# Performance work log

Measured on AMD Instinct MI355X. Metric: run time of the kernel, lower is better.

Reference implementation:

```python
import jax, jax.numpy as jnp
import numpy as np

N_NODES = 100000
N_EDGES = 1600000
N_FEAT = 128
N_CLASSES = 10
N_GRAPHS = 256


def setup_inputs() -> dict:
    key = jax.random.key(0)
    ks = jax.random.split(key, 16)
    x = jax.random.normal(ks[0], (N_NODES, N_FEAT), dtype=jnp.float32)
    edge_index = jax.random.randint(ks[1], (2, N_EDGES), 0, N_NODES, dtype=jnp.int64)
    batch = jnp.sort(jax.random.randint(ks[2], (N_NODES,), 0, N_GRAPHS, dtype=jnp.int64))
    s = 0.1
    # GAT1: in=128 -> heads=8, out_per_head=8, concat -> 64
    W1 = jax.random.normal(ks[3], (N_FEAT, 64), dtype=jnp.float32) * s
    a_src1 = jax.random.normal(ks[4], (8, 8), dtype=jnp.float32) * s
    a_dst1 = jax.random.normal(ks[5], (8, 8), dtype=jnp.float32) * s
    b1 = jnp.zeros((64,), jnp.float32)
    # GAT2: in=64 -> heads=1, out=128
    W2 = jax.random.normal(ks[6], (64, 128), dtype=jnp.float32) * s
    a_src2 = jax.random.normal(ks[7], (1, 128), dtype=jnp.float32) * s
    a_dst2 = jax.random.normal(ks[8], (1, 128), dtype=jnp.float32) * s
    b2 = jnp.zeros((128,), jnp.float32)
    fc_w = jax.random.normal(ks[9], (128, N_CLASSES), dtype=jnp.float32) * s
    fc_b = jnp.zeros((N_CLASSES,), jnp.float32)
    return {"x": x, "edge_index": edge_index, "batch": batch,
            "W1": W1, "a_src1": a_src1, "a_dst1": a_dst1, "b1": b1,
            "W2": W2, "a_src2": a_src2, "a_dst2": a_dst2, "b2": b2,
            "fc_w": fc_w, "fc_b": fc_b}


def _segment_softmax(e, seg, n):
    # e: [E, H]; softmax over edges sharing the same destination node
    m = jax.ops.segment_max(e, seg, num_segments=n)
    m = jnp.where(jnp.isfinite(m), m, jnp.zeros_like(m))  # guard isolated nodes
    ex = jnp.exp(e - m[seg])
    s = jax.ops.segment_sum(ex, seg, num_segments=n)
    return ex / (s[seg] + jnp.asarray(1e-16, e.dtype))


def _gat_conv(x, src, dst, W, a_src, a_dst, bias):
    # PyG GATConv (eval mode, self-loops already appended to src/dst)
    H, C = a_src.shape
    n = x.shape[0]
    h = (x @ W).reshape(n, H, C)                      # [N,H,C]
    al_s = jnp.einsum('nhc,hc->nh', h, a_src)          # [N,H]
    al_d = jnp.einsum('nhc,hc->nh', h, a_dst)
    e = jax.nn.leaky_relu(al_s[src] + al_d[dst], 0.2)  # [E,H]
    alpha = _segment_softmax(e, dst, n)                # [E,H]
    out = jax.ops.segment_sum(h[src] * alpha[..., None], dst, num_segments=n)  # [N,H,C]
    return out.reshape(n, H * C) + bias                # concat=True (H=1 layer2 is identity reshape)


def reference(x, edge_index, batch, W1, a_src1, a_dst1, b1, W2, a_src2, a_dst2, b2, fc_w, fc_b):
    n = x.shape[0]
    loop = jnp.arange(n, dtype=edge_index.dtype)
    src = jnp.concatenate([edge_index[0], loop])       # add self-loops (PyG default)
    dst = jnp.concatenate([edge_index[1], loop])
    x1 = jax.nn.relu(_gat_conv(x, src, dst, W1, a_src1, a_dst1, b1))
    # dropout p=0.6 is identity in eval mode
    x2 = _gat_conv(x1, src, dst, W2, a_src2, a_dst2, b2)
    cnt = jax.ops.segment_sum(jnp.ones((n,), x2.dtype), batch, num_segments=N_GRAPHS)
    pooled = jax.ops.segment_sum(x2, batch, num_segments=N_GRAPHS) / jnp.maximum(cnt, 1.0)[:, None]
    logits = pooled @ fc_w + fc_b
    return jax.nn.log_softmax(logits, axis=1)
```

## Files before the change

### kernel.cpp

```cpp
#include <hip/hip_runtime.h>
#include <math.h>

typedef unsigned int uint;
typedef unsigned short ushort;
typedef unsigned char uchar;
typedef __attribute__((ext_vector_type(2))) float v2f;

#define S1 4.0f
#define S2 16.0f

template <bool HI>
__device__ inline v2f fp8x2f(uint u) {
    return __builtin_amdgcn_cvt_pk_f32_fp8((int)u, HI);
}

__global__ __launch_bounds__(256) void k_gemm1(const float* __restrict__ x,
                                               const float* __restrict__ W1,
                                               const float* __restrict__ as1,
                                               const float* __restrict__ ad1,
                                               uchar* __restrict__ h1f8,
                                               float* __restrict__ al1s,
                                               float* __restrict__ al1d, int N) {
    __shared__ float sB[128 * 64];
    __shared__ float sA[64 * 68];
    const int t = threadIdx.x;
    const int n0 = blockIdx.x * 64;
    {
        const float4* w4 = (const float4*)W1;
        float4* s4 = (float4*)sB;
#pragma unroll
        for (int i = 0; i < 8; ++i) s4[t + i * 256] = w4[t + i * 256];
    }
    const int r0 = (t >> 3) * 2;
    const int c0 = (t & 7) * 8;
    float acc0[8] = {0, 0, 0, 0, 0, 0, 0, 0};
    float acc1[8] = {0, 0, 0, 0, 0, 0, 0, 0};
    for (int kb = 0; kb < 2; ++kb) {
        __syncthreads();
#pragma unroll
        for (int i = 0; i < 4; ++i) {
            int idx = t + i * 256;
            int r = idx >> 4, kc = idx & 15;
            int n = n0 + r;
            float4 v = make_float4(0.f, 0.f, 0.f, 0.f);
            if (n < N) v = ((const float4*)x)[(size_t)n * 32 + kb * 16 + kc];
            *(float4*)&sA[r * 68 + kc * 4] = v;
        }
        __syncthreads();
        const float* bptr = &sB[kb * 64 * 64];
#pragma unroll 8
        for (int kk = 0; kk < 64; ++kk) {
            float a0 = sA[r0 * 68 + kk];
            float a1 = sA[(r0 + 1) * 68 + kk];
            const float* bp = &bptr[kk * 64 + c0];
            float4 b0 = *(const float4*)bp;
            float4 b1v = *(const float4*)(bp + 4);
            acc0[0] += a0 * b0.x; acc0[1] += a0 * b0.y; acc0[2] += a0 * b0.z; acc0[3] += a0 * b0.w;
            acc0[4] += a0 * b1v.x; acc0[5] += a0 * b1v.y; acc0[6] += a0 * b1v.z; acc0[7] += a0 * b1v.w;
            acc1[0] += a1 * b0.x; acc1[1] += a1 * b0.y; acc1[2] += a1 * b0.z; acc1[3] += a1 * b0.w;
            acc1[4] += a1 * b1v.x; acc1[5] += a1 * b1v.y; acc1[6] += a1 * b1v.z; acc1[7] += a1 * b1v.w;
        }
    }
    float ps0 = 0.f, pd0 = 0.f, ps1 = 0.f, pd1 = 0.f;
#pragma unroll
    for (int i = 0; i < 8; ++i) {
        float ws = as1[c0 + i], wd = ad1[c0 + i];
        ps0 += acc0[i] * ws; pd0 += acc0[i] * wd;
        ps1 += acc1[i] * ws; pd1 += acc1[i] * wd;
    }
    int n = n0 + r0;
    int head = t & 7;
    if (n < N) {
        int q0 = 0, q1 = 0;
        q0 = __builtin_amdgcn_cvt_pk_fp8_f32(acc0[0] * S1, acc0[1] * S1, q0, false);
        q0 = __builtin_amdgcn_cvt_pk_fp8_f32(acc0[2] * S1, acc0[3] * S1, q0, true);
        q1 = __builtin_amdgcn_cvt_pk_fp8_f32(acc0[4] * S1, acc0[5] * S1, q1, false);
        q1 = __builtin_amdgcn_cvt_pk_fp8_f32(acc0[6] * S1, acc0[7] * S1, q1, true);
        uint2 p; p.x = (uint)q0; p.y = (uint)q1;
        *(uint2*)&h1f8[(size_t)n * 64 + c0] = p;
        al1s[(size_t)n * 8 + head] = ps0;
        al1d[(size_t)n * 8 + head] = pd0;
    }
    if (n + 1 < N) {
        int q0 = 0, q1 = 0;
        q0 = __builtin_amdgcn_cvt_pk_fp8_f32(acc1[0] * S1, acc1[1] * S1, q0, false);
        q0 = __builtin_amdgcn_cvt_pk_fp8_f32(acc1[2] * S1, acc1[3] * S1, q0, true);
        q1 = __builtin_amdgcn_cvt_pk_fp8_f32(acc1[4] * S1, acc1[5] * S1, q1, false);
        q1 = __builtin_amdgcn_cvt_pk_fp8_f32(acc1[6] * S1, acc1[7] * S1, q1, true);
        uint2 p; p.x = (uint)q0; p.y = (uint)q1;
        *(uint2*)&h1f8[(size_t)(n + 1) * 64 + c0] = p;
        al1s[(size_t)(n + 1) * 8 + head] = ps1;
        al1d[(size_t)(n + 1) * 8 + head] = pd1;
    }
}

__global__ __launch_bounds__(256) void k_gemm2(const float* __restrict__ x1pre,
                                               const float* __restrict__ W2,
                                               const float* __restrict__ b1,
                                               const float* __restrict__ as2,
                                               const float* __restrict__ ad2,
                                               uchar* __restrict__ h2f8,
                                               float* __restrict__ al2s,
                                               float* __restrict__ al2d, int N) {
    __shared__ float sB[64 * 128];
    __shared__ float sA[64 * 68];
    const int t = threadIdx.x;
    const int n0 = blockIdx.x * 64;
    {
        const float4* w4 = (const float4*)W2;
        float4* s4 = (float4*)sB;
#pragma unroll
        for (int i = 0; i < 8; ++i) s4[t + i * 256] = w4[t + i * 256];
    }
#pragma unroll
    for (int i = 0; i < 4; ++i) {
        int idx = t + i * 256;
        int r = idx >> 4, kc = idx & 15;
        int n = n0 + r;
        float4 v = make_float4(0.f, 0.f, 0.f, 0.f);
        if (n < N) {
            v = ((const float4*)x1pre)[(size_t)n * 16 + kc];
            float4 bb = ((const float4*)b1)[kc];
            v.x = fmaxf(v.x + bb.x, 0.f);
            v.y = fmaxf(v.y + bb.y, 0.f);
            v.z = fmaxf(v.z + bb.z, 0.f);
            v.w = fmaxf(v.w + bb.w, 0.f);
        }
        *(float4*)&sA[r * 68 + kc * 4] = v;
    }
    __syncthreads();
    const int r0 = (t >> 3) * 2;
    const int cb = (t & 7) * 4;
    float acc0[16], acc1[16];
#pragma unroll
    for (int i = 0; i < 16; ++i) { acc0[i] = 0.f; acc1[i] = 0.f; }
#pragma unroll 4
    for (int k = 0; k < 64; ++k) {
        float a0 = sA[r0 * 68 + k];
        float a1 = sA[(r0 + 1) * 68 + k];
#pragma unroll
        for (int j = 0; j < 4; ++j) {
            float4 b = *(const float4*)&sB[k * 128 + cb + 32 * j];
            acc0[j * 4 + 0] += a0 * b.x; acc0[j * 4 + 1] += a0 * b.y;
            acc0[j * 4 + 2] += a0 * b.z; acc0[j * 4 + 3] += a0 * b.w;
            acc1[j * 4 + 0] += a1 * b.x; acc1[j * 4 + 1] += a1 * b.y;
            acc1[j * 4 + 2] += a1 * b.z; acc1[j * 4 + 3] += a1 * b.w;
        }
    }
    float ps0 = 0.f, pd0 = 0.f, ps1 = 0.f, pd1 = 0.f;
#pragma unroll
    for (int j = 0; j < 4; ++j)
#pragma unroll
        for (int i = 0; i < 4; ++i) {
            int cc = cb + 32 * j + i;
            float ws = as2[cc], wd = ad2[cc];
            ps0 += acc0[j * 4 + i] * ws; pd0 += acc0[j * 4 + i] * wd;
            ps1 += acc1[j * 4 + i] * ws; pd1 += acc1[j * 4 + i] * wd;
        }
#pragma unroll
    for (int off = 1; off < 8; off <<= 1) {
        ps0 += __shfl_xor(ps0, off); pd0 += __shfl_xor(pd0, off);
        ps1 += __shfl_xor(ps1, off); pd1 += __shfl_xor(pd1, off);
    }
    int n = n0 + r0;
    if (n < N) {
#pragma unroll
        for (int j = 0; j < 4; ++j) {
            int q = 0;
            q = __builtin_amdgcn_cvt_pk_fp8_f32(acc0[j * 4 + 0] * S2, acc0[j * 4 + 1] * S2, q, false);
            q = __builtin_amdgcn_cvt_pk_fp8_f32(acc0[j * 4 + 2] * S2, acc0[j * 4 + 3] * S2, q, true);
            *(uint*)&h2f8[(size_t)n * 128 + cb + 32 * j] = (uint)q;
        }
        if ((t & 7) == 0) { al2s[n] = ps0; al2d[n] = pd0; }
    }
    if (n + 1 < N) {
#pragma unroll
        for (int j = 0; j < 4; ++j) {
            int q = 0;
            q = __builtin_amdgcn_cvt_pk_fp8_f32(acc1[j * 4 + 0] * S2, acc1[j * 4 + 1] * S2, q, false);
            q = __builtin_amdgcn_cvt_pk_fp8_f32(acc1[j * 4 + 2] * S2, acc1[j * 4 + 3] * S2, q, true);
            *(uint*)&h2f8[(size_t)(n + 1) * 128 + cb + 32 * j] = (uint)q;
        }
        if ((t & 7) == 0) { al2s[n + 1] = ps1; al2d[n + 1] = pd1; }
    }
}


__global__ __launch_bounds__(256) void k_hist(const int* __restrict__ dst,
                                              int* __restrict__ counts,
                                              int E, int CH, int NB) {
    __shared__ int hist[784];
    int t = threadIdx.x, b = blockIdx.x;
    for (int k = t; k < NB; k += 256) hist[k] = 0;
    __syncthreads();
    int e0 = b * CH;
    int e1 = e0 + CH; if (e1 > E) e1 = E;
    for (int e = e0 + t; e < e1; e += 256)
        atomicAdd(&hist[dst[e] >> 7], 1);
    __syncthreads();
    for (int k = t; k < NB; k += 256) counts[(size_t)b * NB + k] = hist[k];
}

__global__ __launch_bounds__(256) void k_bscan(int* __restrict__ counts,
                                               int* __restrict__ btot,
                                               int C, int NB) {
    __shared__ int sh[256];
    int t = threadIdx.x, k = blockIdx.x;
    int v[4];
#pragma unroll
    for (int i = 0; i < 4; ++i) {
        int b = t * 4 + i;
        v[i] = (b < C) ? counts[(size_t)b * NB + k] : 0;
    }
    int s = v[0] + v[1] + v[2] + v[3];
    sh[t] = s;
    __syncthreads();
    int accv = s;
    for (int off = 1; off < 256; off <<= 1) {
        int u = (t >= off) ? sh[t - off] : 0;
        __syncthreads();
        accv += u;
        sh[t] = accv;
        __syncthreads();
    }
    int excl = accv - s;
#pragma unroll
    for (int i = 0; i < 4; ++i) {
        int b = t * 4 + i;
        if (b < C) counts[(size_t)b * NB + k] = excl;
        excl += v[i];
    }
    if (t == 255) btot[k] = accv;
}

__global__ void k_bscan2(const int* __restrict__ btot, int* __restrict__ bbase,
                         int NB, int E) {
    __shared__ int sh[1024];
    int t = threadIdx.x;
    int v = (t < NB) ? btot[t] : 0;
    sh[t] = v;
    __syncthreads();
    int accv = v;
    for (int off = 1; off < 1024; off <<= 1) {
        int u = (t >= off) ? sh[t - off] : 0;
        __syncthreads();
        accv += u;
        sh[t] = accv;
        __syncthreads();
    }
    if (t < NB) bbase[t] = accv - v;
    if (t == 0) bbase[NB] = E;
}

__global__ __launch_bounds__(256) void k_bucket(const int* __restrict__ src,
                                                const int* __restrict__ dst,
                                                const int* __restrict__ counts,
                                                const int* __restrict__ bbase,
                                                int* __restrict__ ebuf,
                                                int E, int CH, int NB) {
    __shared__ int pos[784];
    int t = threadIdx.x, b = blockIdx.x;
    for (int k = t; k < NB; k += 256)
        pos[k] = bbase[k] + counts[(size_t)b * NB + k];
    __syncthreads();
    int e0 = b * CH;
    int e1 = e0 + CH; if (e1 > E) e1 = E;
    for (int e = e0 + t; e < e1; e += 256) {
        int d = dst[e], s = src[e];
        int p = atomicAdd(&pos[d >> 7], 1);
        ebuf[p] = (int)((uint)s | ((uint)(d & 127) << 25));
    }
}

__global__ __launch_bounds__(256) void k_csr(const int* __restrict__ bbase,
                                             const int* __restrict__ ebuf,
                                             int* __restrict__ row_ptr,
                                             int* __restrict__ col,
                                             int N, int E) {
    __shared__ int cnt[128];
    __shared__ int fill[128];
    __shared__ int rowb[128];
    __shared__ int sh[256];
    int t = threadIdx.x, k = blockIdx.x;
    int lo = bbase[k], hi = bbase[k + 1];
    int nlo = k << 7;
    int nn = N - nlo; if (nn > 128) nn = 128;
    if (t < 128) { cnt[t] = 0; fill[t] = 0; }
    __syncthreads();
    for (int i = lo + t; i < hi; i += 256)
        atomicAdd(&cnt[((uint)ebuf[i]) >> 25], 1);
    __syncthreads();
    int v = (t < nn) ? (cnt[t] + 1) : 0;
    sh[t] = v;
    __syncthreads();
    int accv = v;
    for (int off = 1; off < 256; off <<= 1) {
        int u = (t >= off) ? sh[t - off] : 0;
        __syncthreads();
        accv += u;
        sh[t] = accv;
        __syncthreads();
    }
    int fbase = lo + nlo;
    if (t < nn) {
        int rb = fbase + accv - v;
        rowb[t] = rb;
        row_ptr[nlo + t] = rb;
        col[rb + cnt[t]] = nlo + t;
    }
    if (k == 0 && t == 0) row_ptr[N] = E + N;
    __syncthreads();
    for (int i = lo + t; i < hi; i += 256) {
        uint e = (uint)ebuf[i];
        int j = (int)(e >> 25);
        int r = atomicAdd(&fill[j], 1);
        col[rowb[j] + r] = (int)(e & 0x1FFFFFFu);
    }
}

__global__ __launch_bounds__(256) void k_edge1(const uchar* __restrict__ h1f8,
                                               const float* __restrict__ al1s,
                                               const float* __restrict__ al1d,
                                               const int* __restrict__ row_ptr,
                                               const int* __restrict__ col,
                                               float* __restrict__ x1pre, int N) {
    int node = blockIdx.x * 4 + (threadIdx.x >> 6);
    if (node >= N) return;
    const int lane = threadIdx.x & 63;
    const int g = lane >> 4;
    const int k4 = lane & 15;
    const int hh = k4 >> 1;
    const uint co = (uint)(k4 * 4);
    const float a_dh = al1d[(((uint)node) << 3) | (uint)hh];
    const int s0 = row_ptr[node], s1 = row_ptr[node + 1];
    float den_part = 0.f;
    v2f accL = {0.f, 0.f};
    v2f accH = {0.f, 0.f};
    for (int base = s0; base < s1; base += 64) {
        int cnt = s1 - base; if (cnt > 64) cnt = 64;
        int cntR = (cnt + 3) & ~3;
        int i = 0;
        for (; i + 16 <= cntR; i += 16) {
            int eA = base + i + g, eB = eA + 4, eC = eA + 8, eD = eA + 12;
            int xD = eD < s1 ? eD : s1 - 1;
            int cA = col[eA], cB = col[eB], cC = col[eC], cD = col[xD];
            uint hA = *(const uint*)(h1f8 + ((((uint)cA) << 6) | co));
            uint hB = *(const uint*)(h1f8 + ((((uint)cB) << 6) | co));
            uint hC = *(const uint*)(h1f8 + ((((uint)cC) << 6) | co));
            uint hD = *(const uint*)(h1f8 + ((((uint)cD) << 6) | co));
            float lA = al1s[((((uint)cA) << 3) | (uint)hh)] + a_dh;
            float lB = al1s[((((uint)cB) << 3) | (uint)hh)] + a_dh;
            float lC = al1s[((((uint)cC) << 3) | (uint)hh)] + a_dh;
            float lD = al1s[((((uint)cD) << 3) | (uint)hh)] + a_dh;
            lA = lA > 0.f ? lA : 0.2f * lA;
            lB = lB > 0.f ? lB : 0.2f * lB;
            lC = lC > 0.f ? lC : 0.2f * lC;
            lD = lD > 0.f ? lD : 0.2f * lD;
            float wA = __expf(lA);
            float wB = __expf(lB);
            float wC = __expf(lC);
            float wD = (eD < s1) ? __expf(lD) : 0.f;
            den_part += wA + wB + wC + wD;
            v2f wA2 = {wA, wA}, wB2 = {wB, wB}, wC2 = {wC, wC}, wD2 = {wD, wD};
            accL += wA2 * fp8x2f<false>(hA);
            accH += wA2 * fp8x2f<true>(hA);
            accL += wB2 * fp8x2f<false>(hB);
            accH += wB2 * fp8x2f<true>(hB);
            accL += wC2 * fp8x2f<false>(hC);
            accH += wC2 * fp8x2f<true>(hC);
            accL += wD2 * fp8x2f<false>(hD);
            accH += wD2 * fp8x2f<true>(hD);
        }
        int rem = cntR - i;
        if (rem & 8) {
            int eA = base + i + g, eB = eA + 4;
            int xB = eB < s1 ? eB : s1 - 1;
            int cA = col[eA], cB = col[xB];
            uint hA = *(const uint*)(h1f8 + ((((uint)cA) << 6) | co));
            uint hB = *(const uint*)(h1f8 + ((((uint)cB) << 6) | co));
            float lA = al1s[((((uint)cA) << 3) | (uint)hh)] + a_dh;
            float lB = al1s[((((uint)cB) << 3) | (uint)hh)] + a_dh;
            lA = lA > 0.f ? lA : 0.2f * lA;
            lB = lB > 0.f ? lB : 0.2f * lB;
            float wA = __expf(lA);
            float wB = (eB < s1) ? __expf(lB) : 0.f;
            den_part += wA + wB;
            v2f wA2 = {wA, wA}, wB2 = {wB, wB};
            accL += wA2 * fp8x2f<false>(hA);
            accH += wA2 * fp8x2f<true>(hA);
            accL += wB2 * fp8x2f<false>(hB);
            accH += wB2 * fp8x2f<true>(hB);
            i += 8;
        }
        if (rem & 4) {
            int eA = base + i + g;
            int xA = eA < s1 ? eA : s1 - 1;
            int cA = col[xA];
            uint hA = *(const uint*)(h1f8 + ((((uint)cA) << 6) | co));
            float lA = al1s[((((uint)cA) << 3) | (uint)hh)] + a_dh;
            lA = lA > 0.f ? lA : 0.2f * lA;
            float wA = (eA < s1) ? __expf(lA) : 0.f;
            den_part += wA;
            v2f wA2 = {wA, wA};
            accL += wA2 * fp8x2f<false>(hA);
            accH += wA2 * fp8x2f<true>(hA);
        }
    }
    float a0 = accL.x, a1 = accL.y, a2 = accH.x, a3 = accH.y;
    a0 += __shfl_xor(a0, 16); a0 += __shfl_xor(a0, 32);
    a1 += __shfl_xor(a1, 16); a1 += __shfl_xor(a1, 32);
    a2 += __shfl_xor(a2, 16); a2 += __shfl_xor(a2, 32);
    a3 += __shfl_xor(a3, 16); a3 += __shfl_xor(a3, 32);
    den_part += __shfl_xor(den_part, 16);
    den_part += __shfl_xor(den_part, 32);
    if (lane < 16) {
        float invd = 1.f / (den_part * S1);
        ((float4*)x1pre)[(size_t)node * 16 + k4] =
            make_float4(a0 * invd, a1 * invd, a2 * invd, a3 * invd);
    }
}

__global__ __launch_bounds__(256) void k_edge2(const uchar* __restrict__ h2f8,
                                               const float* __restrict__ al2s,
                                               const float* __restrict__ al2d,
                                               const int* __restrict__ row_ptr,
                                               const int* __restrict__ col,
                                               float* __restrict__ x2, int N) {
    int node = blockIdx.x * 4 + (threadIdx.x >> 6);
    if (node >= N) return;
    const int lane = threadIdx.x & 63;
    const int g = lane >> 4;
    const int k8 = lane & 15;
    const uint co = (uint)(k8 * 8);
    const float a_d = al2d[node];
    const int s0 = row_ptr[node], s1 = row_ptr[node + 1];
    v2f acc0 = {0.f, 0.f}, acc1 = {0.f, 0.f}, acc2 = {0.f, 0.f}, acc3 = {0.f, 0.f};
    float den_part = 0.f;
    for (int base = s0; base < s1; base += 64) {
        int cnt = s1 - base; if (cnt > 64) cnt = 64;
        int cntR = (cnt + 3) & ~3;
        int i = 0;
        for (; i + 16 <= cntR; i += 16) {
            int eA = base + i + g, eB = eA + 4, eC = eA + 8, eD = eA + 12;
            int xD = eD < s1 ? eD : s1 - 1;
            int cA = col[eA], cB = col[eB], cC = col[eC], cD = col[xD];
            uint2 hA = *(const uint2*)(h2f8 + ((((uint)cA) << 7) | co));
            uint2 hB = *(const uint2*)(h2f8 + ((((uint)cB) << 7) | co));
            uint2 hC = *(const uint2*)(h2f8 + ((((uint)cC) << 7) | co));
            uint2 hD = *(const uint2*)(h2f8 + ((((uint)cD) << 7) | co));
            float lA = al2s[(uint)cA] + a_d;
            float lB = al2s[(uint)cB] + a_d;
            float lC = al2s[(uint)cC] + a_d;
            float lD = al2s[(uint)cD] + a_d;
            lA = lA > 0.f ? lA : 0.2f * lA;
            lB = lB > 0.f ? lB : 0.2f * lB;
            lC = lC > 0.f ? lC : 0.2f * lC;
            lD = lD > 0.f ? lD : 0.2f * lD;
            float wA = __expf(lA);
            float wB = __expf(lB);
            float wC = __expf(lC);
            float wD = (eD < s1) ? __expf(lD) : 0.f;
            den_part += wA + wB + wC + wD;
            v2f wA2 = {wA, wA}, wB2 = {wB, wB}, wC2 = {wC, wC}, wD2 = {wD, wD};
            acc0 += wA2 * fp8x2f<false>(hA.x);
            acc1 += wA2 * fp8x2f<true>(hA.x);
            acc2 += wA2 * fp8x2f<false>(hA.y);
            acc3 += wA2 * fp8x2f<true>(hA.y);
            acc0 += wB2 * fp8x2f<false>(hB.x);
            acc1 += wB2 * fp8x2f<true>(hB.x);
            acc2 += wB2 * fp8x2f<false>(hB.y);
            acc3 += wB2 * fp8x2f<true>(hB.y);
            acc0 += wC2 * fp8x2f<false>(hC.x);
            acc1 += wC2 * fp8x2f<true>(hC.x);
            acc2 += wC2 * fp8x2f<false>(hC.y);
            acc3 += wC2 * fp8x2f<true>(hC.y);
            acc0 += wD2 * fp8x2f<false>(hD.x);
            acc1 += wD2 * fp8x2f<true>(hD.x);
            acc2 += wD2 * fp8x2f<false>(hD.y);
            acc3 += wD2 * fp8x2f<true>(hD.y);
        }
        int rem = cntR - i;
        if (rem & 8) {
            int eA = base + i + g, eB = eA + 4;
            int xB = eB < s1 ? eB : s1 - 1;
            int cA = col[eA], cB = col[xB];
            uint2 hA = *(const uint2*)(h2f8 + ((((uint)cA) << 7) | co));
            uint2 hB = *(const uint2*)(h2f8 + ((((uint)cB) << 7) | co));
            float lA = al2s[(uint)cA] + a_d;
            float lB = al2s[(uint)cB] + a_d;
            lA = lA > 0.f ? lA : 0.2f * lA;
            lB = lB > 0.f ? lB : 0.2f * lB;
            float wA = __expf(lA);
            float wB = (eB < s1) ? __expf(lB) : 0.f;
            den_part += wA + wB;
            v2f wA2 = {wA, wA}, wB2 = {wB, wB};
            acc0 += wA2 * fp8x2f<false>(hA.x);
            acc1 += wA2 * fp8x2f<true>(hA.x);
            acc2 += wA2 * fp8x2f<false>(hA.y);
            acc3 += wA2 * fp8x2f<true>(hA.y);
            acc0 += wB2 * fp8x2f<false>(hB.x);
            acc1 += wB2 * fp8x2f<true>(hB.x);
            acc2 += wB2 * fp8x2f<false>(hB.y);
            acc3 += wB2 * fp8x2f<true>(hB.y);
            i += 8;
        }
        if (rem & 4) {
            int eA = base + i + g;
            int xA = eA < s1 ? eA : s1 - 1;
            int cA = col[xA];
            uint2 hA = *(const uint2*)(h2f8 + ((((uint)cA) << 7) | co));
            float lA = al2s[(uint)cA] + a_d;
            lA = lA > 0.f ? lA : 0.2f * lA;
            float wA = (eA < s1) ? __expf(lA) : 0.f;
            den_part += wA;
            v2f wA2 = {wA, wA};
            acc0 += wA2 * fp8x2f<false>(hA.x);
            acc1 += wA2 * fp8x2f<true>(hA.x);
            acc2 += wA2 * fp8x2f<false>(hA.y);
            acc3 += wA2 * fp8x2f<true>(hA.y);
        }
    }
    den_part += __shfl_xor(den_part, 16);
    den_part += __shfl_xor(den_part, 32);
    float r0 = acc0.x, r1 = acc0.y, r2 = acc1.x, r3 = acc1.y;
    float r4 = acc2.x, r5 = acc2.y, r6 = acc3.x, r7 = acc3.y;
    r0 += __shfl_xor(r0, 16); r0 += __shfl_xor(r0, 32);
    r1 += __shfl_xor(r1, 16); r1 += __shfl_xor(r1, 32);
    r2 += __shfl_xor(r2, 16); r2 += __shfl_xor(r2, 32);
    r3 += __shfl_xor(r3, 16); r3 += __shfl_xor(r3, 32);
    r4 += __shfl_xor(r4, 16); r4 += __shfl_xor(r4, 32);
    r5 += __shfl_xor(r5, 16); r5 += __shfl_xor(r5, 32);
    r6 += __shfl_xor(r6, 16); r6 += __shfl_xor(r6, 32);
    r7 += __shfl_xor(r7, 16); r7 += __shfl_xor(r7, 32);
    if (lane < 16) {
        float invd = 1.f / (den_part * S2);
        float4* dst = (float4*)(x2 + (size_t)node * 128 + co);
        dst[0] = make_float4(r0 * invd, r1 * invd, r2 * invd, r3 * invd);
        dst[1] = make_float4(r4 * invd, r5 * invd, r6 * invd, r7 * invd);
    }
}

__global__ __launch_bounds__(128) void k_pool(const float* __restrict__ x2,
                                              const int* __restrict__ batch,
                                              float* __restrict__ pooled,
                                              float* __restrict__ cnt, int N) {
    int t = threadIdx.x;
    int nstart = blockIdx.x * 128;
    if (nstart >= N) return;
    int nend = nstart + 128;
    if (nend > N) nend = N;
    float acc = 0.f;
    int cur = batch[nstart];
    int count = 0;
    for (int n = nstart; n < nend; ++n) {
        int g = batch[n];
        if (g != cur) {
            atomicAdd(&pooled[(size_t)cur * 128 + t], acc);
            if (t == 0) atomicAdd(&cnt[cur], (float)count);
            acc = 0.f;
            count = 0;
            cur = g;
        }
        acc += x2[(size_t)n * 128 + t];
        ++count;
    }
    atomicAdd(&pooled[(size_t)cur * 128 + t], acc);
    if (t == 0) atomicAdd(&cnt[cur], (float)count);
}

__global__ __launch_bounds__(64) void k_fc(const float* __restrict__ pooled,
                                           const float* __restrict__ cnt,
                                           const float* __restrict__ b2,
                                           const float* __restrict__ fcw,
                                           const float* __restrict__ fcb,
                                           float* __restrict__ out, int G) {
    int g = blockIdx.x;
    int c = threadIdx.x;
    float2 p = ((const float2*)pooled)[(size_t)g * 64 + c];
    float2 bb = ((const float2*)b2)[c];
    float inv = 1.f / fmaxf(cnt[g], 1.f);
    p.x = p.x * inv + bb.x;
    p.y = p.y * inv + bb.y;
    float l[10];
#pragma unroll
    for (int j = 0; j < 10; ++j)
        l[j] = p.x * fcw[(2 * c) * 10 + j] + p.y * fcw[(2 * c + 1) * 10 + j];
#pragma unroll
    for (int j = 0; j < 10; ++j)
        for (int off = 1; off < 64; off <<= 1) l[j] += __shfl_xor(l[j], off);
    if (c == 0) {
        float lj[10];
        float m = -1e30f;
#pragma unroll
        for (int j = 0; j < 10; ++j) {
            lj[j] = l[j] + fcb[j];
            m = fmaxf(m, lj[j]);
        }
        float s = 0.f;
#pragma unroll
        for (int j = 0; j < 10; ++j) s += expf(lj[j] - m);
        float ls = logf(s);
#pragma unroll
        for (int j = 0; j < 10; ++j) out[(size_t)g * 10 + j] = lj[j] - m - ls;
    }
}

extern "C" void kernel_launch(void* const* d_in, const int* in_sizes, int n_in,
                              void* d_out, int out_size, void* d_ws, size_t ws_size,
                              hipStream_t stream) {
    const float* x     = (const float*)d_in[0];
    const int*   ei    = (const int*)d_in[1];
    const int*   batch = (const int*)d_in[2];
    const float* W1    = (const float*)d_in[3];
    const float* as1   = (const float*)d_in[4];
    const float* ad1   = (const float*)d_in[5];
    const float* b1    = (const float*)d_in[6];
    const float* W2    = (const float*)d_in[7];
    const float* as2   = (const float*)d_in[8];
    const float* ad2   = (const float*)d_in[9];
    const float* b2    = (const float*)d_in[10];
    const float* fcw   = (const float*)d_in[11];
    const float* fcb   = (const float*)d_in[12];
    float* out = (float*)d_out;

    const int N = in_sizes[0] / 128;
    const int E = in_sizes[1] / 2;
    const int G = out_size / 10;
    const int* srcp = ei;
    const int* dstp = ei + E;

    float* wf = (float*)d_ws;
    uchar* h1f8   = (uchar*)wf;
    float* x1pre  = wf + (size_t)N * 16;
    float* x2     = wf;
    uchar* h2f8   = (uchar*)(wf + (size_t)N * 128);
    float* al1s_  = wf + (size_t)N * 160;
    float* al1d_  = wf + (size_t)N * 168;
    float* al2s_  = wf + (size_t)N * 176;
    float* al2d_  = wf + (size_t)N * 177;
    float* pooled = wf + (size_t)N * 178;
    float* cnt    = pooled + (size_t)G * 128;

    const int NB = (N + 127) >> 7;
    const int C  = 1024;
    const int CH = (E + C - 1) / C;

    int* ib = (int*)(((uintptr_t)(cnt + G) + 15) & ~(uintptr_t)15);
    int* ebuf    = ib;
    int* counts  = ib + (size_t)E;
    int* btot    = counts + (size_t)C * NB;
    int* bbase   = btot + NB;
    int* row_ptr = bbase + NB + 1;
    int* col     = row_ptr + N + 1;

    size_t zbytes = ((size_t)G * 128 + G) * sizeof(float);
    (void)hipMemsetAsync(pooled, 0, zbytes, stream);

    const int nb64 = (N + 63) / 64;
    const int nb4  = (N + 3) / 4;
    const int nbP  = (N + 127) / 128;

    k_hist<<<C, 256, 0, stream>>>(dstp, counts, E, CH, NB);
    k_gemm1<<<nb64, 256, 0, stream>>>(x, W1, as1, ad1, h1f8, al1s_, al1d_, N);
    k_bscan<<<NB, 256, 0, stream>>>(counts, btot, C, NB);
    k_bscan2<<<1, 1024, 0, stream>>>(btot, bbase, NB, E);
    k_bucket<<<C, 256, 0, stream>>>(srcp, dstp, counts, bbase, ebuf, E, CH, NB);
    k_csr<<<NB, 256, 0, stream>>>(bbase, ebuf, row_ptr, col, N, E);
    k_edge1<<<nb4, 256, 0, stream>>>(h1f8, al1s_, al1d_, row_ptr, col, x1pre, N);
    k_gemm2<<<nb64, 256, 0, stream>>>(x1pre, W2, b1, as2, ad2, h2f8, al2s_, al2d_, N);
    k_edge2<<<nb4, 256, 0, stream>>>(h2f8, al2s_, al2d_, row_ptr, col, x2, N);
    k_pool<<<nbP, 128, 0, stream>>>(x2, batch, pooled, cnt, N);
    k_fc<<<G, 64, 0, stream>>>(pooled, cnt, b2, fcw, fcb, out, G);
}
```

Measured before the change: 351.2 us.

## Interleave layer-1 features with attention logits, fuse bucket scan, store fp16 intermediates

Packs the fp8 layer-1 features and per-head source/destination logits into one 128-byte record per node, so each edge gather in the first attention pass touches a single cache line instead of two separate arrays. The single-block bucket-base scan is folded into every k_bucket block, which removes one kernel launch at the cost of redundant scan work in each block. Layer outputs x1pre and x2 are stored as fp16 instead of fp32, halving their write and read traffic in exchange for some precision loss.

Measured after the change: 340.9 us. 2.9% less time.

```diff
diff --git a/kernel.cpp b/kernel.cpp
--- a/kernel.cpp
+++ b/kernel.cpp
@@ -5,6 +5,8 @@
 typedef unsigned short ushort;
 typedef unsigned char uchar;
 typedef __attribute__((ext_vector_type(2))) float v2f;
+typedef __attribute__((ext_vector_type(4))) _Float16 h4v;
+typedef __attribute__((ext_vector_type(8))) _Float16 h8v;
 
 #define S1 4.0f
 #define S2 16.0f
@@ -18,9 +20,7 @@
                                                const float* __restrict__ W1,
                                                const float* __restrict__ as1,
                                                const float* __restrict__ ad1,
-                                               uchar* __restrict__ h1f8,
-                                               float* __restrict__ al1s,
-                                               float* __restrict__ al1d, int N) {
+                                               uchar* __restrict__ rec1, int N) {
     __shared__ float sB[128 * 64];
     __shared__ float sA[64 * 68];
     const int t = threadIdx.x;
@@ -77,9 +77,10 @@
         q1 = __builtin_amdgcn_cvt_pk_fp8_f32(acc0[4] * S1, acc0[5] * S1, q1, false);
         q1 = __builtin_amdgcn_cvt_pk_fp8_f32(acc0[6] * S1, acc0[7] * S1, q1, true);
         uint2 p; p.x = (uint)q0; p.y = (uint)q1;
-        *(uint2*)&h1f8[(size_t)n * 64 + c0] = p;
-        al1s[(size_t)n * 8 + head] = ps0;
-        al1d[(size_t)n * 8 + head] = pd0;
+        uchar* rp = rec1 + (size_t)n * 128;
+        *(uint2*)(rp + c0) = p;
+        *(float*)(rp + 64 + head * 4) = ps0;
+        *(float*)(rp + 96 + head * 4) = pd0;
     }
     if (n + 1 < N) {
         int q0 = 0, q1 = 0;
@@ -88,13 +89,14 @@
         q1 = __builtin_amdgcn_cvt_pk_fp8_f32(acc1[4] * S1, acc1[5] * S1, q1, false);
         q1 = __builtin_amdgcn_cvt_pk_fp8_f32(acc1[6] * S1, acc1[7] * S1, q1, true);
         uint2 p; p.x = (uint)q0; p.y = (uint)q1;
-        *(uint2*)&h1f8[(size_t)(n + 1) * 64 + c0] = p;
-        al1s[(size_t)(n + 1) * 8 + head] = ps1;
-        al1d[(size_t)(n + 1) * 8 + head] = pd1;
-    }
-}
-
-__global__ __launch_bounds__(256) void k_gemm2(const float* __restrict__ x1pre,
+        uchar* rp = rec1 + (size_t)(n + 1) * 128;
+        *(uint2*)(rp + c0) = p;
+        *(float*)(rp + 64 + head * 4) = ps1;
+        *(float*)(rp + 96 + head * 4) = pd1;
+    }
+}
+
+__global__ __launch_bounds__(256) void k_gemm2(const _Float16* __restrict__ x1pre,
                                                const float* __restrict__ W2,
                                                const float* __restrict__ b1,
                                                const float* __restrict__ as2,
@@ -119,12 +121,12 @@
         int n = n0 + r;
         float4 v = make_float4(0.f, 0.f, 0.f, 0.f);
         if (n < N) {
-            v = ((const float4*)x1pre)[(size_t)n * 16 + kc];
+            h4v hv = *(const h4v*)(x1pre + (size_t)n * 64 + kc * 4);
             float4 bb = ((const float4*)b1)[kc];
-            v.x = fmaxf(v.x + bb.x, 0.f);
-            v.y = fmaxf(v.y + bb.y, 0.f);
-            v.z = fmaxf(v.z + bb.z, 0.f);
-            v.w = fmaxf(v.w + bb.w, 0.f);
+            v.x = fmaxf((float)hv[0] + bb.x, 0.f);
+            v.y = fmaxf((float)hv[1] + bb.y, 0.f);
+            v.z = fmaxf((float)hv[2] + bb.z, 0.f);
+            v.w = fmaxf((float)hv[3] + bb.w, 0.f);
         }
         *(float4*)&sA[r * 68 + kc * 4] = v;
     }
@@ -233,42 +235,55 @@
     if (t == 255) btot[k] = accv;
 }
 
-__global__ void k_bscan2(const int* __restrict__ btot, int* __restrict__ bbase,
-                         int NB, int E) {
-    __shared__ int sh[1024];
-    int t = threadIdx.x;
-    int v = (t < NB) ? btot[t] : 0;
-    sh[t] = v;
-    __syncthreads();
-    int accv = v;
-    for (int off = 1; off < 1024; off <<= 1) {
+__global__ __launch_bounds__(256) void k_bucket(const int* __restrict__ src,
+                                                const int* __restrict__ dst,
+                                                const int* __restrict__ counts,
+                                                const int* __restrict__ btot,
+                                                int* __restrict__ bbase,
+                                                int* __restrict__ ebuf,
+                                                int E, int CH, int NB) {
+    __shared__ int pos[784];
+    __shared__ int sh[256];
+    __shared__ int bb[784];
+    int t = threadIdx.x, b = blockIdx.x;
+    int v[4];
+#pragma unroll
+    for (int i = 0; i < 4; ++i) {
+        int k = t * 4 + i;
+        v[i] = (k < NB) ? btot[k] : 0;
+    }
+    int s = v[0] + v[1] + v[2] + v[3];
+    sh[t] = s;
+    __syncthreads();
+    int accv = s;
+    for (int off = 1; off < 256; off <<= 1) {
         int u = (t >= off) ? sh[t - off] : 0;
         __syncthreads();
         accv += u;
         sh[t] = accv;
         __syncthreads();
     }
-    if (t < NB) bbase[t] = accv - v;
-    if (t == 0) bbase[NB] = E;
-}
-
-__global__ __launch_bounds__(256) void k_bucket(const int* __restrict__ src,
-                                                const int* __restrict__ dst,
-                                                const int* __restrict__ counts,
-                                                const int* __restrict__ bbase,
-                                                int* __restrict__ ebuf,
-                                                int E, int CH, int NB) {
-    __shared__ int pos[784];
-    int t = threadIdx.x, b = blockIdx.x;
+    int excl = accv - s;
+#pragma unroll
+    for (int i = 0; i < 4; ++i) {
+        int k = t * 4 + i;
+        if (k < NB) bb[k] = excl;
+        excl += v[i];
+    }
+    __syncthreads();
     for (int k = t; k < NB; k += 256)
-        pos[k] = bbase[k] + counts[(size_t)b * NB + k];
+        pos[k] = bb[k] + counts[(size_t)b * NB + k];
+    if (b == 0) {
+        for (int k = t; k < NB; k += 256) bbase[k] = bb[k];
+        if (t == 0) bbase[NB] = E;
+    }
     __syncthreads();
     int e0 = b * CH;
     int e1 = e0 + CH; if (e1 > E) e1 = E;
     for (int e = e0 + t; e < e1; e += 256) {
-        int d = dst[e], s = src[e];
+        int d = dst[e], s2 = src[e];
         int p = atomicAdd(&pos[d >> 7], 1);
-        ebuf[p] = (int)((uint)s | ((uint)(d & 127) << 25));
+        ebuf[p] = (int)((uint)s2 | ((uint)(d & 127) << 25));
     }
 }
 
@@ -318,12 +333,10 @@
     }
 }
 
-__global__ __launch_bounds__(256) void k_edge1(const uchar* __restrict__ h1f8,
-                                               const float* __restrict__ al1s,
-                                               const float* __restrict__ al1d,
+__global__ __launch_bounds__(256) void k_edge1(const uchar* __restrict__ rec1,
                                                const int* __restrict__ row_ptr,
                                                const int* __restrict__ col,
-                                               float* __restrict__ x1pre, int N) {
+                                               _Float16* __restrict__ x1pre, int N) {
     int node = blockIdx.x * 4 + (threadIdx.x >> 6);
     if (node >= N) return;
     const int lane = threadIdx.x & 63;
@@ -331,7 +344,8 @@
     const int k4 = lane & 15;
     const int hh = k4 >> 1;
     const uint co = (uint)(k4 * 4);
-    const float a_dh = al1d[(((uint)node) << 3) | (uint)hh];
+    const uint ao = 64u + (uint)(hh * 4);
+    const float a_dh = *(const float*)(rec1 + (((size_t)node) << 7) + 96 + hh * 4);
     const int s0 = row_ptr[node], s1 = row_ptr[node + 1];
     float den_part = 0.f;
     v2f accL = {0.f, 0.f};
@@ -344,14 +358,18 @@
             int eA = base + i + g, eB = eA + 4, eC = eA + 8, eD = eA + 12;
             int xD = eD < s1 ? eD : s1 - 1;
             int cA = col[eA], cB = col[eB], cC = col[eC], cD = col[xD];
-            uint hA = *(const uint*)(h1f8 + ((((uint)cA) << 6) | co));
-            uint hB = *(const uint*)(h1f8 + ((((uint)cB) << 6) | co));
-            uint hC = *(const uint*)(h1f8 + ((((uint)cC) << 6) | co));
-            uint hD = *(const uint*)(h1f8 + ((((uint)cD) << 6) | co));
-            float lA = al1s[((((uint)cA) << 3) | (uint)hh)] + a_dh;
-            float lB = al1s[((((uint)cB) << 3) | (uint)hh)] + a_dh;
-            float lC = al1s[((((uint)cC) << 3) | (uint)hh)] + a_dh;
-            float lD = al1s[((((uint)cD) << 3) | (uint)hh)] + a_dh;
+            const uchar* rA = rec1 + (((uint)cA) << 7);
+            const uchar* rB = rec1 + (((uint)cB) << 7);
+            const uchar* rC = rec1 + (((uint)cC) << 7);
+            const uchar* rD = rec1 + (((uint)cD) << 7);
+            uint hA = *(const uint*)(rA + co);
+            uint hB = *(const uint*)(rB + co);
+            uint hC = *(const uint*)(rC + co);
+            uint hD = *(const uint*)(rD + co);
+            float lA = *(const float*)(rA + ao) + a_dh;
+            float lB = *(const float*)(rB + ao) + a_dh;
+            float lC = *(const float*)(rC + ao) + a_dh;
+            float lD = *(const float*)(rD + ao) + a_dh;
             lA = lA > 0.f ? lA : 0.2f * lA;
             lB = lB > 0.f ? lB : 0.2f * lB;
             lC = lC > 0.f ? lC : 0.2f * lC;
@@ -376,10 +394,12 @@
             int eA = base + i + g, eB = eA + 4;
             int xB = eB < s1 ? eB : s1 - 1;
             int cA = col[eA], cB = col[xB];
-            uint hA = *(const uint*)(h1f8 + ((((uint)cA) << 6) | co));
-            uint hB = *(const uint*)(h1f8 + ((((uint)cB) << 6) | co));
-            float lA = al1s[((((uint)cA) << 3) | (uint)hh)] + a_dh;
-            float lB = al1s[((((uint)cB) << 3) | (uint)hh)] + a_dh;
+            const uchar* rA = rec1 + (((uint)cA) << 7);
+            const uchar* rB = rec1 + (((uint)cB) << 7);
+            uint hA = *(const uint*)(rA + co);
+            uint hB = *(const uint*)(rB + co);
+            float lA = *(const float*)(rA + ao) + a_dh;
+            float lB = *(const float*)(rB + ao) + a_dh;
             lA = lA > 0.f ? lA : 0.2f * lA;
             lB = lB > 0.f ? lB : 0.2f * lB;
             float wA = __expf(lA);
@@ -396,8 +416,9 @@
             int eA = base + i + g;
             int xA = eA < s1 ? eA : s1 - 1;
             int cA = col[xA];
-            uint hA = *(const uint*)(h1f8 + ((((uint)cA) << 6) | co));
-            float lA = al1s[((((uint)cA) << 3) | (uint)hh)] + a_dh;
+            const uchar* rA = rec1 + (((uint)cA) << 7);
+            uint hA = *(const uint*)(rA + co);
+            float lA = *(const float*)(rA + ao) + a_dh;
             lA = lA > 0.f ? lA : 0.2f * lA;
             float wA = (eA < s1) ? __expf(lA) : 0.f;
             den_part += wA;
@@ -415,8 +436,12 @@
     den_part += __shfl_xor(den_part, 32);
     if (lane < 16) {
         float invd = 1.f / (den_part * S1);
-        ((float4*)x1pre)[(size_t)node * 16 + k4] =
-            make_float4(a0 * invd, a1 * invd, a2 * invd, a3 * invd);
+        h4v o;
+        o[0] = (_Float16)(a0 * invd);
+        o[1] = (_Float16)(a1 * invd);
+        o[2] = (_Float16)(a2 * invd);
+        o[3] = (_Float16)(a3 * invd);
+        *(h4v*)(x1pre + (size_t)node * 64 + co) = o;
     }
 }
 
@@ -425,7 +450,7 @@
                                                const float* __restrict__ al2d,
                                                const int* __restrict__ row_ptr,
                                                const int* __restrict__ col,
-                                               float* __restrict__ x2, int N) {
+                                               _Float16* __restrict__ x2, int N) {
     int node = blockIdx.x * 4 + (threadIdx.x >> 6);
     if (node >= N) return;
     const int lane = threadIdx.x & 63;
@@ -534,13 +559,20 @@
     r7 += __shfl_xor(r7, 16); r7 += __shfl_xor(r7, 32);
     if (lane < 16) {
         float invd = 1.f / (den_part * S2);
-        float4* dst = (float4*)(x2 + (size_t)node * 128 + co);
-        dst[0] = make_float4(r0 * invd, r1 * invd, r2 * invd, r3 * invd);
-        dst[1] = make_float4(r4 * invd, r5 * invd, r6 * invd, r7 * invd);
-    }
-}
-
-__global__ __launch_bounds__(128) void k_pool(const float* __restrict__ x2,
+        h8v o;
+        o[0] = (_Float16)(r0 * invd);
+        o[1] = (_Float16)(r1 * invd);
+        o[2] = (_Float16)(r2 * invd);
+        o[3] = (_Float16)(r3 * invd);
+        o[4] = (_Float16)(r4 * invd);
+        o[5] = (_Float16)(r5 * invd);
+        o[6] = (_Float16)(r6 * invd);
+        o[7] = (_Float16)(r7 * invd);
+        *(h8v*)(x2 + (size_t)node * 128 + co) = o;
+    }
+}
+
+__global__ __launch_bounds__(128) void k_pool(const _Float16* __restrict__ x2,
                                               const int* __restrict__ batch,
                                               float* __restrict__ pooled,
                                               float* __restrict__ cnt, int N) {
@@ -561,7 +593,7 @@
             count = 0;
             cur = g;
         }
-        acc += x2[(size_t)n * 128 + t];
+        acc += (float)x2[(size_t)n * 128 + t];
         ++count;
     }
     atomicAdd(&pooled[(size_t)cur * 128 + t], acc);
@@ -630,12 +662,10 @@
     const int* dstp = ei + E;
 
     float* wf = (float*)d_ws;
-    uchar* h1f8   = (uchar*)wf;
-    float* x1pre  = wf + (size_t)N * 16;
-    float* x2     = wf;
-    uchar* h2f8   = (uchar*)(wf + (size_t)N * 128);
-    float* al1s_  = wf + (size_t)N * 160;
-    float* al1d_  = wf + (size_t)N * 168;
+    uchar*    rec1  = (uchar*)wf;
+    _Float16* x1pre = (_Float16*)(wf + (size_t)N * 32);
+    _Float16* x2    = (_Float16*)wf;
+    uchar*    h2f8  = (uchar*)(wf + (size_t)N * 128);
     float* al2s_  = wf + (size_t)N * 176;
     float* al2d_  = wf + (size_t)N * 177;
     float* pooled = wf + (size_t)N * 178;
@@ -661,12 +691,11 @@
     const int nbP  = (N + 127) / 128;
 
     k_hist<<<C, 256, 0, stream>>>(dstp, counts, E, CH, NB);
-    k_gemm1<<<nb64, 256, 0, stream>>>(x, W1, as1, ad1, h1f8, al1s_, al1d_, N);
+    k_gemm1<<<nb64, 256, 0, stream>>>(x, W1, as1, ad1, rec1, N);
     k_bscan<<<NB, 256, 0, stream>>>(counts, btot, C, NB);
-    k_bscan2<<<1, 1024, 0, stream>>>(btot, bbase, NB, E);
-    k_bucket<<<C, 256, 0, stream>>>(srcp, dstp, counts, bbase, ebuf, E, CH, NB);
+    k_bucket<<<C, 256, 0, stream>>>(srcp, dstp, counts, btot, bbase, ebuf, E, CH, NB);
     k_csr<<<NB, 256, 0, stream>>>(bbase, ebuf, row_ptr, col, N, E);
-    k_edge1<<<nb4, 256, 0, stream>>>(h1f8, al1s_, al1d_, row_ptr, col, x1pre, N);
+    k_edge1<<<nb4, 256, 0, stream>>>(rec1, row_ptr, col, x1pre, N);
     k_gemm2<<<nb64, 256, 0, stream>>>(x1pre, W2, b1, as2, ad2, h2f8, al2s_, al2d_, N);
     k_edge2<<<nb4, 256, 0, stream>>>(h2f8, al2s_, al2d_, row_ptr, col, x2, N);
     k_pool<<<nbP, 128, 0, stream>>>(x2, batch, pooled, cnt, N);
```
